# Kernel tuning notes

Measured on AMD Instinct MI355X. Metric: run time of the kernel, lower is better.

Reference implementation:

```python
import jax, jax.numpy as jnp
import numpy as np

MAX_FRAMES = 12
TOPK = 49
NUM_SAMPLES = 256
SIGMA = 0.05
LN_EPS = 1e-5


def setup_inputs() -> dict:
    key = jax.random.key(0)
    ks = jax.random.split(key, 6)
    B, MF, N, D = 8, MAX_FRAMES, 197, 512
    x = jax.random.normal(ks[0], (B, MF * N, D), dtype=jnp.float32)
    noise = jax.random.normal(ks[1], (B * MF, NUM_SAMPLES, N - 1), dtype=jnp.float32)
    ln_gamma = jnp.ones((D,), jnp.float32)
    ln_beta = jnp.zeros((D,), jnp.float32)
    w_in = jax.random.normal(ks[2], (D, D // 2), dtype=jnp.float32) * 0.02
    w1 = jax.random.normal(ks[3], (D, D // 2), dtype=jnp.float32) * 0.02
    w2 = jax.random.normal(ks[4], (D // 2, 1), dtype=jnp.float32) * 0.02
    return {"x": x, "noise": noise, "ln_gamma": ln_gamma, "ln_beta": ln_beta,
            "w_in": w_in, "w1": w1, "w2": w2}


def reference(x, noise, ln_gamma, ln_beta, w_in, w1, w2):
    B, L, D = x.shape
    N = L // MAX_FRAMES
    xf = x.reshape(B * MAX_FRAMES, N, D)          # (b, N, D)

    # PredictorLG: LayerNorm -> Linear -> GELU (torch GELU is exact erf)
    mu = xf.mean(-1, keepdims=True)
    var = xf.var(-1, keepdims=True)               # biased, matches torch LayerNorm
    hn = (xf - mu) * jax.lax.rsqrt(var + LN_EPS) * ln_gamma + ln_beta
    h = jax.nn.gelu(hn @ w_in, approximate=False)  # (b, N, D/2)
    # concat local features with broadcast global (cls-token) features
    g = jnp.broadcast_to(h[:, :1, :], h.shape)
    cat = jnp.concatenate([h, g], axis=-1)         # (b, N, D)
    score = jnp.tanh(jax.nn.gelu(cat @ w1, approximate=False) @ w2)[..., 0]  # (b, N)

    sp = score[:, 1:]                              # (b, d) spatial scores, d = N-1
    b_eff, ns, d = noise.shape
    pert = sp[:, None, :] + noise * SIGMA          # (b, ns, d)

    # top-k set per sample; sorted ascending (matches torch sort of topk indices)
    order = jnp.argsort(-pert, axis=-1)            # descending by value
    top_sorted = jnp.sort(order[..., :TOPK], axis=-1)  # (b, ns, k)

    # mean of one-hots == scatter-add counts / num_samples (avoids one-hot blowup)
    bi = jnp.arange(b_eff)[:, None, None]
    pos = jnp.arange(TOPK)[None, None, :]
    ind = jnp.zeros((b_eff, TOPK, d), x.dtype).at[bi, pos, top_sorted].add(1.0) / ns

    cls_feat = xf[:, :1, :]                        # (b, 1, D)
    spat_feat = xf[:, 1:, :]                       # (b, d, D)
    sel = jnp.einsum('bkl,bld->bkd', ind, spat_feat)  # (b, k, D)
    out = jnp.concatenate([cls_feat, sel], axis=1)    # (b, 1+k, D)
    return out.reshape(B, MAX_FRAMES * (1 + TOPK), D)
```

## Files before the change

### kernel.cpp

```cpp
#include <hip/hip_runtime.h>
#include <math.h>

#define NFRAME 96
#define NTOK   197
#define NSPAT  196
#define DIM    512
#define DH     256
#define NSAMP  256
#define KSEL   49
#define SIG    0.05f
#define MPAD   208
#define MTOT   (NFRAME * MPAD)

typedef unsigned short u16;
typedef __attribute__((ext_vector_type(8))) short bf16x8;
typedef __attribute__((ext_vector_type(4))) float f32x4;

__device__ __forceinline__ float gelu_exact(float v) {
    return 0.5f * v * (1.0f + erff(v * 0.70710678118654752440f));
}
__device__ __forceinline__ unsigned bf16_rne(float f) {
    unsigned u = __float_as_uint(f);
    return (u + 0x7fffu + ((u >> 16) & 1u)) >> 16;
}
__device__ __forceinline__ float bf16_to_f(unsigned h) {
    return __uint_as_float(h << 16);
}

__global__ __launch_bounds__(256) void k0_prep(
    const float* __restrict__ x, const float* __restrict__ gamma,
    const float* __restrict__ beta,
    const float* __restrict__ w_in, const float* __restrict__ w1,
    u16* __restrict__ wiT_hi, u16* __restrict__ wiT_lo,
    u16* __restrict__ w1T_hi, u16* __restrict__ w1T_lo,
    u16* __restrict__ xs_hi, u16* __restrict__ xs_lo)
{
    if (blockIdx.x < 512) {
        const int n = blockIdx.x & 255, which = blockIdx.x >> 8;
        const float* w = which ? w1 : w_in;
        u16* th = which ? w1T_hi : wiT_hi;
        u16* tl = which ? w1T_lo : wiT_lo;
        for (int k = threadIdx.x; k < DIM; k += 256) {
            float v = w[(size_t)k * DH + n];
            unsigned hi = bf16_rne(v);
            unsigned lo = bf16_rne(v - bf16_to_f(hi));
            th[(size_t)n * DIM + k] = (u16)hi;
            tl[(size_t)n * DIM + k] = (u16)lo;
        }
        return;
    }
    const int row  = (blockIdx.x - 512) * 4 + (threadIdx.x >> 6);
    const int lane = threadIdx.x & 63;
    const int f = row / MPAD;
    int rr = row - f * MPAD; if (rr > NTOK - 1) rr = NTOK - 1;
    const float* xr = x + ((size_t)f * NTOK + rr) * DIM + lane * 8;
    float4 a = *(const float4*)xr, b4 = *(const float4*)(xr + 4);
    float e[8] = {a.x, a.y, a.z, a.w, b4.x, b4.y, b4.z, b4.w};
    float s = 0.f, sq = 0.f;
    #pragma unroll
    for (int j = 0; j < 8; ++j) { s += e[j]; sq += e[j] * e[j]; }
    #pragma unroll
    for (int o = 32; o > 0; o >>= 1) {
        s  += __shfl_xor(s,  o, 64);
        sq += __shfl_xor(sq, o, 64);
    }
    const float mu  = s * (1.f / 512.f);
    const float var = sq * (1.f / 512.f) - mu * mu;
    const float rs  = 1.f / sqrtf(var + 1e-5f);

    const float* gp = gamma + lane * 8;
    const float* bp = beta + lane * 8;
    float4 g0 = *(const float4*)gp, g1 = *(const float4*)(gp + 4);
    float4 b0 = *(const float4*)bp, b1 = *(const float4*)(bp + 4);
    float gg[8] = {g0.x, g0.y, g0.z, g0.w, g1.x, g1.y, g1.z, g1.w};
    float bt[8] = {b0.x, b0.y, b0.z, b0.w, b1.x, b1.y, b1.z, b1.w};

    unsigned hw[4], lw[4];
    #pragma unroll
    for (int p = 0; p < 4; ++p) {
        float s0 = rs * gg[2*p],   s1 = rs * gg[2*p+1];
        float v0 = e[2*p]   * s0 + (bt[2*p]   - mu * s0);
        float v1 = e[2*p+1] * s1 + (bt[2*p+1] - mu * s1);
        unsigned h0 = bf16_rne(v0), h1 = bf16_rne(v1);
        float l0 = v0 - bf16_to_f(h0), l1 = v1 - bf16_to_f(h1);
        hw[p] = h0 | (h1 << 16);
        lw[p] = bf16_rne(l0) | (bf16_rne(l1) << 16);
    }
    size_t off = (size_t)row * DIM + lane * 8;
    *(uint4*)(xs_hi + off) = make_uint4(hw[0], hw[1], hw[2], hw[3]);
    *(uint4*)(xs_lo + off) = make_uint4(lw[0], lw[1], lw[2], lw[3]);
}

#define LDG 40
__global__ __launch_bounds__(256, 4) void k1_gemm1(
    const u16* __restrict__ xs_hi, const u16* __restrict__ xs_lo,
    const u16* __restrict__ wiT_hi, const u16* __restrict__ wiT_lo,
    u16* __restrict__ h_hi, u16* __restrict__ h_lo)
{
    __shared__ u16 Ah[128][LDG], Al[128][LDG], Bh[64][LDG], Bl[64][LDG];
    const int t = threadIdx.x, lane = t & 63, wv = t >> 6;
    const int linear = (blockIdx.x & 7) * 78 + (blockIdx.x >> 3);
    const int Mb = linear >> 2, Nb = linear & 3;
    const int R0 = Mb * 128, N0 = Nb * 64;
    const int wm = wv >> 1, wn = wv & 1;
    const int m15 = lane & 15, q = lane >> 4;

    f32x4 acc[4][2];
    #pragma unroll
    for (int i = 0; i < 4; ++i)
        #pragma unroll
        for (int j = 0; j < 2; ++j)
            acc[i][j] = (f32x4){0.f, 0.f, 0.f, 0.f};

    const int ar = t >> 1, as = (t & 1) * 16;
    const int br = t >> 2, bs = (t & 3) * 8;
    const size_t abase = (size_t)(R0 + ar) * DIM + as;
    const size_t bbase = (size_t)(N0 + br) * DIM + bs;

    uint4 pAh0 = *(const uint4*)(xs_hi + abase);
    uint4 pAh1 = *(const uint4*)(xs_hi + abase + 8);
    uint4 pAl0 = *(const uint4*)(xs_lo + abase);
    uint4 pAl1 = *(const uint4*)(xs_lo + abase + 8);
    uint4 pBh  = *(const uint4*)(wiT_hi + bbase);
    uint4 pBl  = *(const uint4*)(wiT_lo + bbase);

    for (int k0 = 0; k0 < DIM; k0 += 32) {
        __syncthreads();
        *(uint4*)&Ah[ar][as]     = pAh0;
        *(uint4*)&Ah[ar][as + 8] = pAh1;
        *(uint4*)&Al[ar][as]     = pAl0;
        *(uint4*)&Al[ar][as + 8] = pAl1;
        *(uint4*)&Bh[br][bs]     = pBh;
        *(uint4*)&Bl[br][bs]     = pBl;
        if (k0 + 32 < DIM) {
            pAh0 = *(const uint4*)(xs_hi + abase + k0 + 32);
            pAh1 = *(const uint4*)(xs_hi + abase + k0 + 40);
            pAl0 = *(const uint4*)(xs_lo + abase + k0 + 32);
            pAl1 = *(const uint4*)(xs_lo + abase + k0 + 40);
            pBh  = *(const uint4*)(wiT_hi + bbase + k0 + 32);
            pBl  = *(const uint4*)(wiT_lo + bbase + k0 + 32);
        }
        __syncthreads();

        const int ko = q * 8;
        bf16x8 ah[4], al[4], bh[2], bl[2];
        #pragma unroll
        for (int i = 0; i < 4; ++i) {
            ah[i] = *(const bf16x8*)&Ah[wm*64 + i*16 + m15][ko];
            al[i] = *(const bf16x8*)&Al[wm*64 + i*16 + m15][ko];
        }
        #pragma unroll
        for (int i = 0; i < 2; ++i) {
            bh[i] = *(const bf16x8*)&Bh[wn*32 + i*16 + m15][ko];
            bl[i] = *(const bf16x8*)&Bl[wn*32 + i*16 + m15][ko];
        }
        #pragma unroll
        for (int mt = 0; mt < 4; ++mt)
            #pragma unroll
            for (int nt = 0; nt < 2; ++nt) {
                f32x4 c = acc[mt][nt];
                c = __builtin_amdgcn_mfma_f32_16x16x32_bf16(ah[mt], bh[nt], c, 0, 0, 0);
                c = __builtin_amdgcn_mfma_f32_16x16x32_bf16(al[mt], bh[nt], c, 0, 0, 0);
                c = __builtin_amdgcn_mfma_f32_16x16x32_bf16(ah[mt], bl[nt], c, 0, 0, 0);
                acc[mt][nt] = c;
            }
    }

    #pragma unroll
    for (int mt = 0; mt < 4; ++mt)
        #pragma unroll
        for (int nt = 0; nt < 2; ++nt)
            #pragma unroll
            for (int reg = 0; reg < 4; ++reg) {
                int r = R0 + wm*64 + mt*16 + q*4 + reg;
                int c = N0 + wn*32 + nt*16 + m15;
                float v = gelu_exact(acc[mt][nt][reg]);
                unsigned hb = bf16_rne(v);
                unsigned lb = bf16_rne(v - bf16_to_f(hb));
                size_t off = (size_t)r * DH + c;
                h_hi[off] = (u16)hb;
                h_lo[off] = (u16)lb;
            }
}

__global__ __launch_bounds__(256, 4) void k1_gemm2(
    const u16* __restrict__ h_hi, const u16* __restrict__ h_lo,
    const u16* __restrict__ w1T_hi, const u16* __restrict__ w1T_lo,
    const float* __restrict__ w2, float* __restrict__ s_half)
{
    __shared__ u16 Ah[64][LDG], Al[64][LDG], Bh[128][LDG], Bl[128][LDG];
    __shared__ float red[2][2][32];
    const int t = threadIdx.x, lane = t & 63, wv = t >> 6;
    const int linear = (blockIdx.x & 7) * 78 + (blockIdx.x >> 3);
    const int Mb = linear >> 1, Nb = linear & 1;
    const int R0 = Mb * 64, N0 = Nb * 128;
    const int wm = wv >> 1, wn = wv & 1;
    const int m15 = lane & 15, q = lane >> 4;

    f32x4 acc[2][4];
    #pragma unroll
    for (int i = 0; i < 2; ++i)
        #pragma unroll
        for (int j = 0; j < 4; ++j)
            acc[i][j] = (f32x4){0.f, 0.f, 0.f, 0.f};

    const int ar = t >> 2, as = (t & 3) * 8;
    const int agrow = R0 + ar;
    const size_t arow_off = (size_t)agrow * DH;
    const size_t g0_off   = (size_t)((agrow / MPAD) * MPAD) * DH;
    const int br = t >> 1, bs = (t & 1) * 16;
    const size_t bbase = (size_t)(N0 + br) * DIM + bs;

    auto asrc = [&](int k0) -> size_t {
        return (k0 < DH) ? (arow_off + k0 + as) : (g0_off + (k0 - DH) + as);
    };

    uint4 pAh = *(const uint4*)(h_hi + asrc(0));
    uint4 pAl = *(const uint4*)(h_lo + asrc(0));
    uint4 pBh0 = *(const uint4*)(w1T_hi + bbase);
    uint4 pBh1 = *(const uint4*)(w1T_hi + bbase + 8);
    uint4 pBl0 = *(const uint4*)(w1T_lo + bbase);
    uint4 pBl1 = *(const uint4*)(w1T_lo + bbase + 8);

    for (int k0 = 0; k0 < DIM; k0 += 32) {
        __syncthreads();
        *(uint4*)&Ah[ar][as]     = pAh;
        *(uint4*)&Al[ar][as]     = pAl;
        *(uint4*)&Bh[br][bs]     = pBh0;
        *(uint4*)&Bh[br][bs + 8] = pBh1;
        *(uint4*)&Bl[br][bs]     = pBl0;
        *(uint4*)&Bl[br][bs + 8] = pBl1;
        if (k0 + 32 < DIM) {
            size_t srcn = asrc(k0 + 32);
            pAh  = *(const uint4*)(h_hi + srcn);
            pAl  = *(const uint4*)(h_lo + srcn);
            pBh0 = *(const uint4*)(w1T_hi + bbase + k0 + 32);
            pBh1 = *(const uint4*)(w1T_hi + bbase + k0 + 40);
            pBl0 = *(const uint4*)(w1T_lo + bbase + k0 + 32);
            pBl1 = *(const uint4*)(w1T_lo + bbase + k0 + 40);
        }
        __syncthreads();

        const int ko = q * 8;
        bf16x8 ah[2], al[2], bh[4], bl[4];
        #pragma unroll
        for (int i = 0; i < 2; ++i) {
            ah[i] = *(const bf16x8*)&Ah[wm*32 + i*16 + m15][ko];
            al[i] = *(const bf16x8*)&Al[wm*32 + i*16 + m15][ko];
        }
        #pragma unroll
        for (int i = 0; i < 4; ++i) {
            bh[i] = *(const bf16x8*)&Bh[wn*64 + i*16 + m15][ko];
            bl[i] = *(const bf16x8*)&Bl[wn*64 + i*16 + m15][ko];
        }
        #pragma unroll
        for (int mt = 0; mt < 2; ++mt)
            #pragma unroll
            for (int nt = 0; nt < 4; ++nt) {
                f32x4 c = acc[mt][nt];
                c = __builtin_amdgcn_mfma_f32_16x16x32_bf16(ah[mt], bh[nt], c, 0, 0, 0);
                c = __builtin_amdgcn_mfma_f32_16x16x32_bf16(al[mt], bh[nt], c, 0, 0, 0);
                c = __builtin_amdgcn_mfma_f32_16x16x32_bf16(ah[mt], bl[nt], c, 0, 0, 0);
                acc[mt][nt] = c;
            }
    }

    float w2v[4];
    #pragma unroll
    for (int nt = 0; nt < 4; ++nt) w2v[nt] = w2[N0 + wn*64 + nt*16 + m15];
    #pragma unroll
    for (int mt = 0; mt < 2; ++mt)
        #pragma unroll
        for (int reg = 0; reg < 4; ++reg) {
            float s = 0.f;
            #pragma unroll
            for (int nt = 0; nt < 4; ++nt)
                s += gelu_exact(acc[mt][nt][reg]) * w2v[nt];
            #pragma unroll
            for (int o = 1; o <= 8; o <<= 1)
                s += __shfl_xor(s, o, 64);
            if (m15 == 0)
                red[wn][wm][mt*16 + q*4 + reg] = s;
        }
    __syncthreads();
    if (t < 64) {
        int wmj = t >> 5, rl = t & 31;
        float sv = red[0][wmj][rl] + red[1][wmj][rl];
        s_half[(size_t)Nb * MTOT + R0 + t] = sv;
    }
}

__global__ __launch_bounds__(1024) void k2_select(
    const float* __restrict__ s_half, const float* __restrict__ noise,
    int* __restrict__ hist2)
{
    const int fb   = blockIdx.x;
    const int f    = fb >> 1;
    const int half = fb & 1;
    const int t    = threadIdx.x;
    const int lane = t & 63;
    const int wv   = t >> 6;

    __shared__ int hist_s[KSEL * NSPAT];
    for (int i = t; i < KSEL * NSPAT; i += 1024) hist_s[i] = 0;

    const float* sA = s_half;
    const float* sB = s_half + MTOT;
    float spv[4];
    #pragma unroll
    for (int j = 0; j < 4; ++j) {
        int l = lane + 64 * j;
        if (l < NSPAT) {
            size_t idx = (size_t)f * MPAD + 1 + l;
            spv[j] = tanhf(sA[idx] + sB[idx]);
        } else spv[j] = 0.f;
    }
    __syncthreads();

    const unsigned long long lmask = (1ull << lane) - 1ull;

    for (int si = 0; si < 8; ++si) {
        const int s = half * 128 + wv * 8 + si;
        const float* nz = noise + ((size_t)f * NSAMP + s) * NSPAT;
        unsigned key[4];
        #pragma unroll
        for (int j = 0; j < 4; ++j) {
            int l = lane + 64 * j;
            if (l < NSPAT) {
                float p = spv[j] + nz[l] * SIG;
                unsigned u = __float_as_uint(p);
                key[j] = (u & 0x80000000u) ? ~u : (u | 0x80000000u);
            } else {
                key[j] = 0u;
            }
        }

        unsigned ans = 0u;
        for (int bit = 31; bit >= 0; --bit) {
            unsigned cand = ans | (1u << bit);
            int cnt = 0;
            #pragma unroll
            for (int j = 0; j < 4; ++j)
                cnt += __popcll(__ballot(key[j] >= cand));
            if (cnt >= KSEL) ans = cand;
        }

        unsigned long long eq[4];
        int cgt = 0;
        #pragma unroll
        for (int j = 0; j < 4; ++j) {
            cgt += __popcll(__ballot(key[j] > ans));
            eq[j] = __ballot(key[j] == ans);
        }
        const int quota = KSEL - cgt;
        int eqpre[4]; { int run = 0;
            #pragma unroll
            for (int j = 0; j < 4; ++j) { eqpre[j] = run; run += __popcll(eq[j]); } }

        int pre = 0;
        #pragma unroll
        for (int j = 0; j < 4; ++j) {
            bool iseq = (key[j] == ans);
            int trk = eqpre[j] + __popcll(eq[j] & lmask);
            bool selj = (key[j] > ans) || (iseq && trk < quota);
            unsigned long long sb = __ballot(selj);
            int rk = pre + __popcll(sb & lmask);
            if (selj)
                atomicAdd(&hist_s[rk * NSPAT + lane + 64 * j], 1);
            pre += __popcll(sb);
        }
    }

    __syncthreads();
    int* hb = hist2 + (size_t)fb * (KSEL * NSPAT);
    for (int i = t; i < KSEL * NSPAT; i += 1024)
        hb[i] = hist_s[i];
}

__global__ __launch_bounds__(256) void k3_output(
    const float* __restrict__ x, const int* __restrict__ hist2,
    float* __restrict__ out)
{
    const int b  = blockIdx.x >> 2;
    const int ds = blockIdx.x & 3;
    const int d0 = ds * 128;
    const int t  = threadIdx.x;
    const int tdc = t & 31;
    const int tk  = t >> 5;

    __shared__ float hist_s[NSPAT * KSEL + 8];

    const int* h0 = hist2 + (size_t)(2 * b) * (KSEL * NSPAT);
    const int* h1 = h0 + KSEL * NSPAT;
    for (int i = t; i < KSEL * NSPAT; i += 256) {
        int k = i / NSPAT;
        int l = i - k * NSPAT;
        hist_s[l * KSEL + k] = (float)(h0[i] + h1[i]);
    }
    if (t < 128)
        out[(size_t)b * 50 * DIM + d0 + t] = x[(size_t)b * NTOK * DIM + d0 + t];
    __syncthreads();

    const float* xs = x + ((size_t)b * NTOK + 1) * DIM + d0 + tdc * 4;
    float4 acc[7];
    #pragma unroll
    for (int i = 0; i < 7; ++i) acc[i] = make_float4(0.f, 0.f, 0.f, 0.f);

    #pragma unroll 2
    for (int l = 0; l < NSPAT; ++l) {
        float4 v = *(const float4*)(xs + (size_t)l * DIM);
        const float* hl = &hist_s[l * KSEL + tk];
        #pragma unroll
        for (int i = 0; i < 7; ++i) {
            float w = hl[8 * i];
            acc[i].x += w * v.x; acc[i].y += w * v.y;
            acc[i].z += w * v.z; acc[i].w += w * v.w;
        }
    }

    const float inv = 1.f / 256.f;
    #pragma unroll
    for (int i = 0; i < 7; ++i) {
        int k = tk + 8 * i;
        if (k < KSEL) {
            float4 o = make_float4(acc[i].x * inv, acc[i].y * inv,
                                   acc[i].z * inv, acc[i].w * inv);
            *(float4*)&out[((size_t)b * 50 + 1 + k) * DIM + d0 + tdc * 4] = o;
        }
    }
}

extern "C" void kernel_launch(void* const* d_in, const int* in_sizes, int n_in,
                              void* d_out, int out_size, void* d_ws, size_t ws_size,
                              hipStream_t stream)
{
    const float* x     = (const float*)d_in[0];
    const float* noise = (const float*)d_in[1];
    const float* gamma = (const float*)d_in[2];
    const float* beta  = (const float*)d_in[3];
    const float* w_in  = (const float*)d_in[4];
    const float* w1    = (const float*)d_in[5];
    const float* w2    = (const float*)d_in[6];
    float* out = (float*)d_out;

    char* ws = (char*)d_ws;
    int*   hist2   = (int*)  (ws + 0);
    float* s_half  = (float*)(ws + 7375872);
    u16*   wiT_hi  = (u16*)  (ws + 7535616);
    u16*   wiT_lo  = (u16*)  (ws + 7797760);
    u16*   w1T_hi  = (u16*)  (ws + 8059904);
    u16*   w1T_lo  = (u16*)  (ws + 8322048);
    u16*   h_hi    = (u16*)  (ws + 8584192);
    u16*   h_lo    = (u16*)  (ws + 18807808);
    u16*   xs_hi   = (u16*)  (ws + 29031424);
    u16*   xs_lo   = (u16*)  (ws + 49478656);

    k0_prep<<<512 + MTOT / 4, 256, 0, stream>>>(x, gamma, beta, w_in, w1,
                                                wiT_hi, wiT_lo, w1T_hi, w1T_lo,
                                                xs_hi, xs_lo);
    k1_gemm1<<<(MTOT / 128) * 4, 256, 0, stream>>>(xs_hi, xs_lo, wiT_hi, wiT_lo,
                                                   h_hi, h_lo);
    k1_gemm2<<<(MTOT / 64) * 2, 256, 0, stream>>>(h_hi, h_lo, w1T_hi, w1T_lo,
                                                  w2, s_half);
    k2_select<<<NFRAME * 2, 1024, 0, stream>>>(s_half, noise, hist2);
    k3_output<<<NFRAME * 4, 256, 0, stream>>>(x, hist2, out);
}
```

Baseline: 234.1 us.

## Fuse top-k histogram selection and weighted gather into one per-frame kernel

Merges the selection kernel and the output kernel into a single kernel with one 1024-thread block per frame. Each block processes all 256 samples, keeps the histogram in shared memory, transposes it to a padded float layout, and computes the weighted sum over x directly. This removes the global histogram round-trip and one launch. The cost is half as many blocks for selection (96 instead of 192) and fewer blocks for the gather (96 instead of 384), so parallelism and occupancy drop on a large GPU.

```diff
diff --git a/kernel.cpp b/kernel.cpp
--- a/kernel.cpp
+++ b/kernel.cpp
@@ -11,6 +11,7 @@
 #define SIG    0.05f
 #define MPAD   208
 #define MTOT   (NFRAME * MPAD)
+#define KP3    52
 
 typedef unsigned short u16;
 typedef __attribute__((ext_vector_type(8))) short bf16x8;
@@ -290,19 +291,19 @@
     }
 }
 
-__global__ __launch_bounds__(1024) void k2_select(
+__global__ __launch_bounds__(1024) void k23_fused(
     const float* __restrict__ s_half, const float* __restrict__ noise,
-    int* __restrict__ hist2)
+    const float* __restrict__ x, float* __restrict__ out)
 {
-    const int fb   = blockIdx.x;
-    const int f    = fb >> 1;
-    const int half = fb & 1;
+    const int f    = blockIdx.x;
     const int t    = threadIdx.x;
     const int lane = t & 63;
     const int wv   = t >> 6;
 
-    __shared__ int hist_s[KSEL * NSPAT];
-    for (int i = t; i < KSEL * NSPAT; i += 1024) hist_s[i] = 0;
+    __shared__ int   hist_i[KSEL * NSPAT];
+    __shared__ float hist_f[NSPAT * KP3];
+
+    for (int i = t; i < KSEL * NSPAT; i += 1024) hist_i[i] = 0;
 
     const float* sA = s_half;
     const float* sB = s_half + MTOT;
@@ -319,8 +320,8 @@
 
     const unsigned long long lmask = (1ull << lane) - 1ull;
 
-    for (int si = 0; si < 8; ++si) {
-        const int s = half * 128 + wv * 8 + si;
+    for (int si = 0; si < 16; ++si) {
+        const int s = wv * 16 + si;
         const float* nz = noise + ((size_t)f * NSAMP + s) * NSPAT;
         unsigned key[4];
         #pragma unroll
@@ -366,50 +367,32 @@
             unsigned long long sb = __ballot(selj);
             int rk = pre + __popcll(sb & lmask);
             if (selj)
-                atomicAdd(&hist_s[rk * NSPAT + lane + 64 * j], 1);
+                atomicAdd(&hist_i[rk * NSPAT + lane + 64 * j], 1);
             pre += __popcll(sb);
         }
     }
 
     __syncthreads();
-    int* hb = hist2 + (size_t)fb * (KSEL * NSPAT);
-    for (int i = t; i < KSEL * NSPAT; i += 1024)
-        hb[i] = hist_s[i];
-}
-
-__global__ __launch_bounds__(256) void k3_output(
-    const float* __restrict__ x, const int* __restrict__ hist2,
-    float* __restrict__ out)
-{
-    const int b  = blockIdx.x >> 2;
-    const int ds = blockIdx.x & 3;
-    const int d0 = ds * 128;
-    const int t  = threadIdx.x;
-    const int tdc = t & 31;
-    const int tk  = t >> 5;
-
-    __shared__ float hist_s[NSPAT * KSEL + 8];
-
-    const int* h0 = hist2 + (size_t)(2 * b) * (KSEL * NSPAT);
-    const int* h1 = h0 + KSEL * NSPAT;
-    for (int i = t; i < KSEL * NSPAT; i += 256) {
-        int k = i / NSPAT;
-        int l = i - k * NSPAT;
-        hist_s[l * KSEL + k] = (float)(h0[i] + h1[i]);
-    }
-    if (t < 128)
-        out[(size_t)b * 50 * DIM + d0 + t] = x[(size_t)b * NTOK * DIM + d0 + t];
+
+    for (int i = t; i < NSPAT * KP3; i += 1024) {
+        int l = i / KP3, k = i - l * KP3;
+        hist_f[i] = (k < KSEL) ? (float)hist_i[k * NSPAT + l] : 0.f;
+    }
+    if (t < DIM)
+        out[(size_t)f * 50 * DIM + t] = x[(size_t)f * NTOK * DIM + t];
     __syncthreads();
 
-    const float* xs = x + ((size_t)b * NTOK + 1) * DIM + d0 + tdc * 4;
+    const int tdc = t & 127;
+    const int tk  = t >> 7;
+    const float* xs = x + ((size_t)f * NTOK + 1) * DIM + tdc * 4;
     float4 acc[7];
     #pragma unroll
     for (int i = 0; i < 7; ++i) acc[i] = make_float4(0.f, 0.f, 0.f, 0.f);
 
-    #pragma unroll 2
+    #pragma unroll 7
     for (int l = 0; l < NSPAT; ++l) {
         float4 v = *(const float4*)(xs + (size_t)l * DIM);
-        const float* hl = &hist_s[l * KSEL + tk];
+        const float* hl = &hist_f[l * KP3 + tk];
         #pragma unroll
         for (int i = 0; i < 7; ++i) {
             float w = hl[8 * i];
@@ -425,7 +408,7 @@
         if (k < KSEL) {
             float4 o = make_float4(acc[i].x * inv, acc[i].y * inv,
                                    acc[i].z * inv, acc[i].w * inv);
-            *(float4*)&out[((size_t)b * 50 + 1 + k) * DIM + d0 + tdc * 4] = o;
+            *(float4*)&out[((size_t)f * 50 + 1 + k) * DIM + tdc * 4] = o;
         }
     }
 }
@@ -444,16 +427,15 @@
     float* out = (float*)d_out;
 
     char* ws = (char*)d_ws;
-    int*   hist2   = (int*)  (ws + 0);
-    float* s_half  = (float*)(ws + 7375872);
-    u16*   wiT_hi  = (u16*)  (ws + 7535616);
-    u16*   wiT_lo  = (u16*)  (ws + 7797760);
-    u16*   w1T_hi  = (u16*)  (ws + 8059904);
-    u16*   w1T_lo  = (u16*)  (ws + 8322048);
-    u16*   h_hi    = (u16*)  (ws + 8584192);
-    u16*   h_lo    = (u16*)  (ws + 18807808);
-    u16*   xs_hi   = (u16*)  (ws + 29031424);
-    u16*   xs_lo   = (u16*)  (ws + 49478656);
+    float* s_half  = (float*)(ws + 0);
+    u16*   wiT_hi  = (u16*)  (ws + 159744);
+    u16*   wiT_lo  = (u16*)  (ws + 421888);
+    u16*   w1T_hi  = (u16*)  (ws + 684032);
+    u16*   w1T_lo  = (u16*)  (ws + 946176);
+    u16*   h_hi    = (u16*)  (ws + 1208320);
+    u16*   h_lo    = (u16*)  (ws + 11431936);
+    u16*   xs_hi   = (u16*)  (ws + 21655552);
+    u16*   xs_lo   = (u16*)  (ws + 42102784);
 
     k0_prep<<<512 + MTOT / 4, 256, 0, stream>>>(x, gamma, beta, w_in, w1,
                                                 wiT_hi, wiT_lo, w1T_hi, w1T_lo,
@@ -462,6 +444,5 @@
                                                    h_hi, h_lo);
     k1_gemm2<<<(MTOT / 64) * 2, 256, 0, stream>>>(h_hi, h_lo, w1T_hi, w1T_lo,
                                                   w2, s_half);
-    k2_select<<<NFRAME * 2, 1024, 0, stream>>>(s_half, noise, hist2);
-    k3_output<<<NFRAME * 4, 256, 0, stream>>>(x, hist2, out);
-}
+    k23_fused<<<NFRAME, 1024, 0, stream>>>(s_half, noise, x, out);
+}
```

Result: slower. 263.9 us (+12.7%).
